# Kernel tuning notes

Hardware: AMD Instinct MI355X
Metric: run time of the kernel (lower is better)

Reference implementation:

```python
import jax, jax.numpy as jnp
import numpy as np

B, H, W, C = 32, 64, 64, 256


def setup_inputs() -> dict:
    key = jax.random.key(0)
    kq, kk, kv = jax.random.split(key, 3)
    query = jax.random.normal(kq, (B, H, W, C), dtype=jnp.float32)
    keys = jax.random.normal(kk, (B, H, W, C), dtype=jnp.float32)
    values = jax.random.normal(kv, (B, H, W, C), dtype=jnp.float32)
    return {"query": query, "keys": keys, "values": values}


def reference(query, keys, values):
    # A[b,q,k] = sum_{h,w} query[b,h,w,q] * keys[b,h,w,k]
    scores = jnp.einsum("bhwq,bhwk->bqk", query, keys)
    attn = jax.nn.softmax(scores, axis=-1)  # softmax over keys axis
    # out[b,q,h,w] = sum_k attn[b,q,k] * values[b,h,w,k]
    out = jnp.einsum("bqk,bhwk->bqhw", attn, values)
    return out
```

## Files before the change

kernel.cpp:

```cpp
#include <hip/hip_runtime.h>
#include <hip/hip_bf16.h>

#define B_  32
#define HW_ 4096
#define C_  256
#define S_LDS 40

using bf16x8 = __attribute__((ext_vector_type(8))) short;
using f32x4  = __attribute__((ext_vector_type(4))) float;
using u32x4  = __attribute__((ext_vector_type(4))) uint;

__device__ __forceinline__ ushort f2bf_rn(float x) {
    uint u = __builtin_bit_cast(uint, x);
    u += 0x7FFFu + ((u >> 16) & 1u);
    return (ushort)(u >> 16);
}
__device__ __forceinline__ uint pk_bf2(float a, float b) {
    return ((uint)f2bf_rn(b) << 16) | (uint)f2bf_rn(a);
}
__device__ __forceinline__ uint pk_rtz(float x0, float x1) {
    return __builtin_amdgcn_perm(__builtin_bit_cast(uint, x1),
                                 __builtin_bit_cast(uint, x0), 0x07060302u);
}
__device__ __forceinline__ void split2_rtz(float x0, float x1, uint& hi2, uint& lo2) {
    uint u0 = __builtin_bit_cast(uint, x0), u1 = __builtin_bit_cast(uint, x1);
    hi2 = __builtin_amdgcn_perm(u1, u0, 0x07060302u);
    float h0 = __builtin_bit_cast(float, u0 & 0xFFFF0000u);
    float h1 = __builtin_bit_cast(float, u1 & 0xFFFF0000u);
    lo2 = pk_rtz(x0 - h0, x1 - h1);
}

__global__ __launch_bounds__(256, 3) void scores_kernel(const float* __restrict__ qg,
                                                        const float* __restrict__ kg,
                                                        float* __restrict__ dst,
                                                        long slabStride) {
    int x  = blockIdx.x;
    int s  = x & 3;
    int tn = (x >> 2) & 3;
    int tm = (x >> 4) & 1;
    int b  = x >> 5;

    __shared__ __align__(16) ushort Qhi[128 * S_LDS], Qlo[128 * S_LDS];
    __shared__ __align__(16) ushort Khi[64 * S_LDS],  Klo[64 * S_LDS];

    int tid = threadIdx.x, lane = tid & 63, w = tid >> 6;
    int m0 = (w >> 1) * 64;
    int n0 = (w & 1) * 32;
    int g = lane >> 4, r16 = lane & 15;

    int cq = tid & 127;
    int hq = (tid >> 7) * 16;
    int ck = tid & 63;
    int hk = (tid >> 6) * 8;

    const float* qcol = qg + (size_t)b * HW_ * C_ + tm * 128 + cq;
    const float* kcol = kg + (size_t)b * HW_ * C_ + tn * 64 + ck;

    f32x4 acc[4][2];
#pragma unroll
    for (int i = 0; i < 4; ++i)
#pragma unroll
        for (int j = 0; j < 2; ++j) acc[i][j] = (f32x4){0.f, 0.f, 0.f, 0.f};

#define LOAD_QK(qr, kr, itv) {                                                 \
        int hw0 = s * 1024 + (itv) * 32;                                       \
        const float* qp = qcol + (size_t)(hw0 + hq) * C_;                      \
        _Pragma("unroll")                                                      \
        for (int j = 0; j < 16; ++j) qr[j] = qp[(size_t)j * C_];               \
        const float* kp = kcol + (size_t)(hw0 + hk) * C_;                      \
        _Pragma("unroll")                                                      \
        for (int j = 0; j < 8; ++j) kr[j] = kp[(size_t)j * C_];                \
    }

#define CONVERT_STORE(qr, kr) {                                                \
        uint qh[8], ql[8];                                                     \
        _Pragma("unroll")                                                      \
        for (int p = 0; p < 8; ++p) split2_rtz(qr[2*p], qr[2*p+1], qh[p], ql[p]); \
        int qb_ = cq * S_LDS + hq;                                             \
        *reinterpret_cast<u32x4*>(&Qhi[qb_])     = (u32x4){qh[0], qh[1], qh[2], qh[3]}; \
        *reinterpret_cast<u32x4*>(&Qhi[qb_ + 8]) = (u32x4){qh[4], qh[5], qh[6], qh[7]}; \
        *reinterpret_cast<u32x4*>(&Qlo[qb_])     = (u32x4){ql[0], ql[1], ql[2], ql[3]}; \
        *reinterpret_cast<u32x4*>(&Qlo[qb_ + 8]) = (u32x4){ql[4], ql[5], ql[6], ql[7]}; \
        uint kh[4], kl[4];                                                     \
        _Pragma("unroll")                                                      \
        for (int p = 0; p < 4; ++p) split2_rtz(kr[2*p], kr[2*p+1], kh[p], kl[p]); \
        int kb_ = ck * S_LDS + hk;                                             \
        *reinterpret_cast<u32x4*>(&Khi[kb_]) = (u32x4){kh[0], kh[1], kh[2], kh[3]}; \
        *reinterpret_cast<u32x4*>(&Klo[kb_]) = (u32x4){kl[0], kl[1], kl[2], kl[3]}; \
    }

#define MFMA_PHASE() {                                                         \
        __builtin_amdgcn_s_setprio(1);                                         \
        bf16x8 ahi[4], alo[4];                                                 \
        _Pragma("unroll")                                                      \
        for (int mi = 0; mi < 4; ++mi) {                                       \
            int off = (m0 + mi * 16 + r16) * S_LDS + g * 8;                    \
            ahi[mi] = *reinterpret_cast<const bf16x8*>(&Qhi[off]);             \
            alo[mi] = *reinterpret_cast<const bf16x8*>(&Qlo[off]);             \
        }                                                                      \
        _Pragma("unroll")                                                      \
        for (int ni = 0; ni < 2; ++ni) {                                       \
            int off = (n0 + ni * 16 + r16) * S_LDS + g * 8;                    \
            bf16x8 bhi = *reinterpret_cast<const bf16x8*>(&Khi[off]);          \
            bf16x8 blo = *reinterpret_cast<const bf16x8*>(&Klo[off]);          \
            _Pragma("unroll")                                                  \
            for (int mi = 0; mi < 4; ++mi) {                                   \
                acc[mi][ni] = __builtin_amdgcn_mfma_f32_16x16x32_bf16(ahi[mi], bhi, acc[mi][ni], 0, 0, 0); \
                acc[mi][ni] = __builtin_amdgcn_mfma_f32_16x16x32_bf16(ahi[mi], blo, acc[mi][ni], 0, 0, 0); \
                acc[mi][ni] = __builtin_amdgcn_mfma_f32_16x16x32_bf16(alo[mi], bhi, acc[mi][ni], 0, 0, 0); \
            }                                                                  \
        }                                                                      \
        __builtin_amdgcn_s_setprio(0);                                         \
    }

#define STEP(qc, kc, qn, kn, itload, doload) {                                 \
        if (doload) LOAD_QK(qn, kn, itload);                                   \
        __syncthreads();                                                       \
        CONVERT_STORE(qc, kc);                                                 \
        __syncthreads();                                                       \
        MFMA_PHASE();                                                          \
    }

    float qa[16], qb[16], qc[16], ka[8], kb[8], kc[8];
    LOAD_QK(qa, ka, 0);
    LOAD_QK(qb, kb, 1);
    for (int p = 0; p < 10; ++p) {
        STEP(qa, ka, qc, kc, 3 * p + 2, true);
        STEP(qb, kb, qa, ka, 3 * p + 3, true);
        STEP(qc, kc, qb, kb, 3 * p + 4, true);
    }
    STEP(qa, ka, qb, kb, 0, false);
    STEP(qb, kb, qa, ka, 0, false);

    float* base = dst + (size_t)s * slabStride;
#pragma unroll
    for (int mi = 0; mi < 4; ++mi)
#pragma unroll
        for (int ni = 0; ni < 2; ++ni)
#pragma unroll
            for (int r = 0; r < 4; ++r) {
                int qrow = tm * 128 + m0 + mi * 16 + g * 4 + r;
                int kc2  = tn * 64 + n0 + ni * 16 + r16;
                float* p = base + ((size_t)b * 256 + qrow) * 256 + kc2;
                if (slabStride) *p = acc[mi][ni][r];
                else            atomicAdd(p, acc[mi][ni][r]);
            }
#undef STEP
#undef MFMA_PHASE
#undef CONVERT_STORE
#undef LOAD_QK
}

__global__ __launch_bounds__(256) void softmax_kernel(const float* __restrict__ scores,
                                                      ushort* __restrict__ attn,
                                                      int nslab, long slabStride) {
    int wid  = blockIdx.x * 4 + (threadIdx.x >> 6);
    int lane = threadIdx.x & 63;
    const float* p0 = scores + (size_t)wid * 256 + lane * 4;
    float4 v = *reinterpret_cast<const float4*>(p0);
    for (int sl = 1; sl < nslab; ++sl) {
        const float4 t = *reinterpret_cast<const float4*>(p0 + (size_t)sl * slabStride);
        v.x += t.x; v.y += t.y; v.z += t.z; v.w += t.w;
    }
    float m = fmaxf(fmaxf(v.x, v.y), fmaxf(v.z, v.w));
#pragma unroll
    for (int off = 32; off; off >>= 1) m = fmaxf(m, __shfl_xor(m, off, 64));
    float e0 = __expf(v.x - m), e1 = __expf(v.y - m), e2 = __expf(v.z - m), e3 = __expf(v.w - m);
    float ssum = e0 + e1 + e2 + e3;
#pragma unroll
    for (int off = 32; off; off >>= 1) ssum += __shfl_xor(ssum, off, 64);
    float inv = 1.0f / ssum;
    uint2 o;
    o.x = pk_bf2(e0 * inv, e1 * inv);
    o.y = pk_bf2(e2 * inv, e3 * inv);
    *reinterpret_cast<uint2*>(attn + (size_t)wid * 256 + lane * 4) = o;
}

__global__ __launch_bounds__(256, 4) void pv_kernel(const ushort* __restrict__ attn,
                                                    const float* __restrict__ vg,
                                                    float* __restrict__ out) {
    int b   = blockIdx.x >> 6;
    int hw0 = (blockIdx.x & 63) * 64;
    int tid = threadIdx.x, lane = tid & 63, w = tid >> 6;
    int m0  = w * 64;
    int g   = lane >> 4, r16 = lane & 15;

    __shared__ __align__(16) float Vt[2 * 64 * 32];

    int srow = tid >> 2;
    int sslot = (tid & 3) * 2;
    int wi0 = srow * 32 + ((sslot ^ (srow & 7)) * 4);
    int wi1 = srow * 32 + (((sslot + 1) ^ (srow & 7)) * 4);
    const float* vstage = vg + ((size_t)(b * HW_ + hw0 + srow)) * C_ + sslot * 4;

    const ushort* abase = attn + (size_t)b * 256 * 256 + g * 8;

    f32x4 acc[4][4];
#pragma unroll
    for (int i = 0; i < 4; ++i)
#pragma unroll
        for (int j = 0; j < 4; ++j) acc[i][j] = (f32x4){0.f, 0.f, 0.f, 0.f};

    {
        f32x4 p0 = *reinterpret_cast<const f32x4*>(vstage);
        f32x4 p1 = *reinterpret_cast<const f32x4*>(vstage + 4);
        *reinterpret_cast<f32x4*>(&Vt[wi0]) = p0;
        *reinterpret_cast<f32x4*>(&Vt[wi1]) = p1;
    }
    __syncthreads();

    for (int p = 0; p < 8; ++p) {
        float* rbuf = &Vt[(p & 1) * 64 * 32];
        float* wbuf = &Vt[((p + 1) & 1) * 64 * 32];

        f32x4 n0v, n1v;
        if (p < 7) {
            n0v = *reinterpret_cast<const f32x4*>(vstage + (p + 1) * 32);
            n1v = *reinterpret_cast<const f32x4*>(vstage + (p + 1) * 32 + 4);
        }

        int k0 = p * 32;
        bf16x8 a[4];
#pragma unroll
        for (int mi = 0; mi < 4; ++mi)
            a[mi] = *reinterpret_cast<const bf16x8*>(abase + (size_t)(m0 + mi * 16 + r16) * 256 + k0);

#pragma unroll
        for (int ni = 0; ni < 4; ++ni) {
            int row = ni * 16 + r16, key = row & 7;
            f32x4 f0 = *reinterpret_cast<const f32x4*>(&rbuf[row * 32 + (((2 * g)     ^ key) * 4)]);
            f32x4 f1 = *reinterpret_cast<const f32x4*>(&rbuf[row * 32 + (((2 * g + 1) ^ key) * 4)]);
            bf16x8 bf = __builtin_bit_cast(bf16x8, (u32x4){
                pk_rtz(f0[0], f0[1]), pk_rtz(f0[2], f0[3]),
                pk_rtz(f1[0], f1[1]), pk_rtz(f1[2], f1[3])});
#pragma unroll
            for (int mi = 0; mi < 4; ++mi)
                acc[mi][ni] = __builtin_amdgcn_mfma_f32_16x16x32_bf16(a[mi], bf, acc[mi][ni], 0, 0, 0);
        }

        if (p < 7) {
            *reinterpret_cast<f32x4*>(&wbuf[wi0]) = n0v;
            *reinterpret_cast<f32x4*>(&wbuf[wi1]) = n1v;
            __syncthreads();
        }
    }

#pragma unroll
    for (int mi = 0; mi < 4; ++mi)
#pragma unroll
        for (int ni = 0; ni < 4; ++ni)
#pragma unroll
            for (int r = 0; r < 4; ++r) {
                int qrow = m0 + mi * 16 + g * 4 + r;
                int hw   = hw0 + ni * 16 + r16;
                out[((size_t)b * 256 + qrow) * 4096 + hw] = acc[mi][ni][r];
            }
}

extern "C" void kernel_launch(void* const* d_in, const int* in_sizes, int n_in,
                              void* d_out, int out_size, void* d_ws, size_t ws_size,
                              hipStream_t stream) {
    const float* q = (const float*)d_in[0];
    const float* k = (const float*)d_in[1];
    const float* v = (const float*)d_in[2];
    float* out = (float*)d_out;

    const size_t slab = (size_t)B_ * 256 * 256;
    const size_t needBytes = 4 * slab * 4 + slab * 2;
    float* scores = (float*)d_ws;

    if (ws_size >= needBytes) {
        ushort* attn = (ushort*)((char*)d_ws + 4 * slab * 4);
        scores_kernel<<<1024, 256, 0, stream>>>(q, k, scores, (long)slab);
        softmax_kernel<<<2048, 256, 0, stream>>>(scores, attn, 4, (long)slab);
        pv_kernel<<<2048, 256, 0, stream>>>(attn, v, out);
    } else {
        ushort* attn = (ushort*)((char*)d_ws + slab * 4);
        (void)hipMemsetAsync(d_ws, 0, slab * 4, stream);
        scores_kernel<<<1024, 256, 0, stream>>>(q, k, scores, 0L);
        softmax_kernel<<<2048, 256, 0, stream>>>(scores, attn, 1, 0L);
        pv_kernel<<<2048, 256, 0, stream>>>(attn, v, out);
    }
}
```

Measured before the change: 176.9 us.

## Load MFMA fragments straight from global memory, dropping the LDS staging in scores kernel

The scores kernel no longer stages converted Q/K tiles through shared memory behind two barriers per step. Each lane now loads its MFMA operand fragments directly from global memory, splits them into bf16 hi/lo in registers and issues the MFMAs. This removes the LDS traffic, the barriers and the manual triple-buffered prefetch. In exchange, Q and K elements shared by both waves along a dimension are fetched redundantly from global or L2 memory. Software pipelining of loads is lost, and the accesses are 16-lane strided scalar loads that coalesce less well.

```diff
diff --git a/kernel.cpp b/kernel.cpp
--- a/kernel.cpp
+++ b/kernel.cpp
@@ -4,7 +4,6 @@
 #define B_  32
 #define HW_ 4096
 #define C_  256
-#define S_LDS 40
 
 using bf16x8 = __attribute__((ext_vector_type(8))) short;
 using f32x4  = __attribute__((ext_vector_type(4))) float;
@@ -40,21 +39,13 @@
     int tm = (x >> 4) & 1;
     int b  = x >> 5;
 
-    __shared__ __align__(16) ushort Qhi[128 * S_LDS], Qlo[128 * S_LDS];
-    __shared__ __align__(16) ushort Khi[64 * S_LDS],  Klo[64 * S_LDS];
-
     int tid = threadIdx.x, lane = tid & 63, w = tid >> 6;
     int m0 = (w >> 1) * 64;
     int n0 = (w & 1) * 32;
     int g = lane >> 4, r16 = lane & 15;
 
-    int cq = tid & 127;
-    int hq = (tid >> 7) * 16;
-    int ck = tid & 63;
-    int hk = (tid >> 6) * 8;
-
-    const float* qcol = qg + (size_t)b * HW_ * C_ + tm * 128 + cq;
-    const float* kcol = kg + (size_t)b * HW_ * C_ + tn * 64 + ck;
+    const float* qbase = qg + (size_t)b * HW_ * C_ + tm * 128 + m0 + r16;
+    const float* kbase = kg + (size_t)b * HW_ * C_ + tn * 64 + n0 + r16;
 
     f32x4 acc[4][2];
 #pragma unroll
@@ -62,75 +53,49 @@
 #pragma unroll
         for (int j = 0; j < 2; ++j) acc[i][j] = (f32x4){0.f, 0.f, 0.f, 0.f};
 
-#define LOAD_QK(qr, kr, itv) {                                                 \
-        int hw0 = s * 1024 + (itv) * 32;                                       \
-        const float* qp = qcol + (size_t)(hw0 + hq) * C_;                      \
-        _Pragma("unroll")                                                      \
-        for (int j = 0; j < 16; ++j) qr[j] = qp[(size_t)j * C_];               \
-        const float* kp = kcol + (size_t)(hw0 + hk) * C_;                      \
-        _Pragma("unroll")                                                      \
-        for (int j = 0; j < 8; ++j) kr[j] = kp[(size_t)j * C_];                \
-    }
-
-#define CONVERT_STORE(qr, kr) {                                                \
-        uint qh[8], ql[8];                                                     \
-        _Pragma("unroll")                                                      \
-        for (int p = 0; p < 8; ++p) split2_rtz(qr[2*p], qr[2*p+1], qh[p], ql[p]); \
-        int qb_ = cq * S_LDS + hq;                                             \
-        *reinterpret_cast<u32x4*>(&Qhi[qb_])     = (u32x4){qh[0], qh[1], qh[2], qh[3]}; \
-        *reinterpret_cast<u32x4*>(&Qhi[qb_ + 8]) = (u32x4){qh[4], qh[5], qh[6], qh[7]}; \
-        *reinterpret_cast<u32x4*>(&Qlo[qb_])     = (u32x4){ql[0], ql[1], ql[2], ql[3]}; \
-        *reinterpret_cast<u32x4*>(&Qlo[qb_ + 8]) = (u32x4){ql[4], ql[5], ql[6], ql[7]}; \
-        uint kh[4], kl[4];                                                     \
-        _Pragma("unroll")                                                      \
-        for (int p = 0; p < 4; ++p) split2_rtz(kr[2*p], kr[2*p+1], kh[p], kl[p]); \
-        int kb_ = ck * S_LDS + hk;                                             \
-        *reinterpret_cast<u32x4*>(&Khi[kb_]) = (u32x4){kh[0], kh[1], kh[2], kh[3]}; \
-        *reinterpret_cast<u32x4*>(&Klo[kb_]) = (u32x4){kl[0], kl[1], kl[2], kl[3]}; \
-    }
-
-#define MFMA_PHASE() {                                                         \
-        __builtin_amdgcn_s_setprio(1);                                         \
-        bf16x8 ahi[4], alo[4];                                                 \
-        _Pragma("unroll")                                                      \
-        for (int mi = 0; mi < 4; ++mi) {                                       \
-            int off = (m0 + mi * 16 + r16) * S_LDS + g * 8;                    \
-            ahi[mi] = *reinterpret_cast<const bf16x8*>(&Qhi[off]);             \
-            alo[mi] = *reinterpret_cast<const bf16x8*>(&Qlo[off]);             \
-        }                                                                      \
-        _Pragma("unroll")                                                      \
-        for (int ni = 0; ni < 2; ++ni) {                                       \
-            int off = (n0 + ni * 16 + r16) * S_LDS + g * 8;                    \
-            bf16x8 bhi = *reinterpret_cast<const bf16x8*>(&Khi[off]);          \
-            bf16x8 blo = *reinterpret_cast<const bf16x8*>(&Klo[off]);          \
-            _Pragma("unroll")                                                  \
-            for (int mi = 0; mi < 4; ++mi) {                                   \
-                acc[mi][ni] = __builtin_amdgcn_mfma_f32_16x16x32_bf16(ahi[mi], bhi, acc[mi][ni], 0, 0, 0); \
-                acc[mi][ni] = __builtin_amdgcn_mfma_f32_16x16x32_bf16(ahi[mi], blo, acc[mi][ni], 0, 0, 0); \
-                acc[mi][ni] = __builtin_amdgcn_mfma_f32_16x16x32_bf16(alo[mi], bhi, acc[mi][ni], 0, 0, 0); \
-            }                                                                  \
-        }                                                                      \
-        __builtin_amdgcn_s_setprio(0);                                         \
-    }
-
-#define STEP(qc, kc, qn, kn, itload, doload) {                                 \
-        if (doload) LOAD_QK(qn, kn, itload);                                   \
-        __syncthreads();                                                       \
-        CONVERT_STORE(qc, kc);                                                 \
-        __syncthreads();                                                       \
-        MFMA_PHASE();                                                          \
-    }
-
-    float qa[16], qb[16], qc[16], ka[8], kb[8], kc[8];
-    LOAD_QK(qa, ka, 0);
-    LOAD_QK(qb, kb, 1);
-    for (int p = 0; p < 10; ++p) {
-        STEP(qa, ka, qc, kc, 3 * p + 2, true);
-        STEP(qb, kb, qa, ka, 3 * p + 3, true);
-        STEP(qc, kc, qb, kb, 3 * p + 4, true);
-    }
-    STEP(qa, ka, qb, kb, 0, false);
-    STEP(qb, kb, qa, ka, 0, false);
+    for (int it = 0; it < 32; ++it) {
+        int hwb = s * 1024 + it * 32 + g * 8;
+        const float* qp = qbase + (size_t)hwb * C_;
+        const float* kp = kbase + (size_t)hwb * C_;
+
+        float qv[4][8], kv[2][8];
+#pragma unroll
+        for (int j = 0; j < 8; ++j) {
+#pragma unroll
+            for (int mi = 0; mi < 4; ++mi) qv[mi][j] = qp[(size_t)j * C_ + mi * 16];
+#pragma unroll
+            for (int ni = 0; ni < 2; ++ni) kv[ni][j] = kp[(size_t)j * C_ + ni * 16];
+        }
+
+        bf16x8 ahi[4], alo[4], bhi[2], blo[2];
+#pragma unroll
+        for (int mi = 0; mi < 4; ++mi) {
+            uint h[4], l[4];
+#pragma unroll
+            for (int p = 0; p < 4; ++p) split2_rtz(qv[mi][2 * p], qv[mi][2 * p + 1], h[p], l[p]);
+            ahi[mi] = __builtin_bit_cast(bf16x8, (u32x4){h[0], h[1], h[2], h[3]});
+            alo[mi] = __builtin_bit_cast(bf16x8, (u32x4){l[0], l[1], l[2], l[3]});
+        }
+#pragma unroll
+        for (int ni = 0; ni < 2; ++ni) {
+            uint h[4], l[4];
+#pragma unroll
+            for (int p = 0; p < 4; ++p) split2_rtz(kv[ni][2 * p], kv[ni][2 * p + 1], h[p], l[p]);
+            bhi[ni] = __builtin_bit_cast(bf16x8, (u32x4){h[0], h[1], h[2], h[3]});
+            blo[ni] = __builtin_bit_cast(bf16x8, (u32x4){l[0], l[1], l[2], l[3]});
+        }
+
+        __builtin_amdgcn_s_setprio(1);
+#pragma unroll
+        for (int ni = 0; ni < 2; ++ni)
+#pragma unroll
+            for (int mi = 0; mi < 4; ++mi) {
+                acc[mi][ni] = __builtin_amdgcn_mfma_f32_16x16x32_bf16(ahi[mi], bhi[ni], acc[mi][ni], 0, 0, 0);
+                acc[mi][ni] = __builtin_amdgcn_mfma_f32_16x16x32_bf16(ahi[mi], blo[ni], acc[mi][ni], 0, 0, 0);
+                acc[mi][ni] = __builtin_amdgcn_mfma_f32_16x16x32_bf16(alo[mi], bhi[ni], acc[mi][ni], 0, 0, 0);
+            }
+        __builtin_amdgcn_s_setprio(0);
+    }
 
     float* base = dst + (size_t)s * slabStride;
 #pragma unroll
@@ -145,10 +110,6 @@
                 if (slabStride) *p = acc[mi][ni][r];
                 else            atomicAdd(p, acc[mi][ni][r]);
             }
-#undef STEP
-#undef MFMA_PHASE
-#undef CONVERT_STORE
-#undef LOAD_QK
 }
 
 __global__ __launch_bounds__(256) void softmax_kernel(const float* __restrict__ scores,
```

Result: slower. 200.1 us (+13.1%).
